# Kernel optimization log

Measured on AMD Instinct MI355X. Metric: run time of the kernel, lower is better.

## Reference

```python
import jax, jax.numpy as jnp
import numpy as np
import math

B, H, W, C = 8, 112, 112, 192
WS, SHIFT, NH = 7, 3, 6
HD = C // NH
N = WS * WS
NW = (H // WS) * (W // WS)
MLP_HID = 4 * C
LOG100 = math.log(100.0)


def _rel_table():
    ch = np.arange(-(WS - 1), WS, dtype=np.float32)
    t = np.stack(np.meshgrid(ch, ch, indexing='ij')).transpose(1, 2, 0).reshape(-1, 2)
    t = t / float(WS - 1) * 8.0
    t = np.sign(t) * np.log2(np.abs(t) + 1.0) / np.log2(8.0)
    return t.astype(np.float32)  # ((2*WS-1)^2, 2)


def _rel_index():
    coords = np.stack(np.meshgrid(np.arange(WS), np.arange(WS), indexing='ij')).reshape(2, -1)
    rel = (coords[:, :, None] - coords[:, None, :]).transpose(1, 2, 0)
    rel = rel + np.array([WS - 1, WS - 1])
    rel = rel * np.array([2 * WS - 1, 1])
    return rel.sum(-1).astype(np.int32)  # (N, N)


def _attn_mask():
    img = np.zeros((H, W), dtype=np.float32)
    cnt = 0
    for hsl in (slice(0, -WS), slice(-WS, -SHIFT), slice(-SHIFT, None)):
        for wsl in (slice(0, -WS), slice(-WS, -SHIFT), slice(-SHIFT, None)):
            img[hsl, wsl] = cnt
            cnt += 1
    mw = img.reshape(H // WS, WS, W // WS, WS).transpose(0, 2, 1, 3).reshape(-1, N)
    diff = mw[:, None, :] - mw[:, :, None]
    return np.where(diff != 0, -100.0, 0.0).astype(np.float32)  # (NW, N, N)

REL_TABLE = jnp.asarray(_rel_table())
REL_INDEX = jnp.asarray(_rel_index())
ATTN_MASK = jnp.asarray(_attn_mask())


def _ln(v, g, b, eps=1e-5):
    m = jnp.mean(v, axis=-1, keepdims=True)
    s = jnp.mean((v - m) ** 2, axis=-1, keepdims=True)
    return (v - m) / jnp.sqrt(s + eps) * g + b


def setup_inputs() -> dict:
    key = jax.random.key(0)
    ks = jax.random.split(key, 12)
    std = 0.02
    inp = {
        'x': jax.random.normal(ks[0], (B, H * W, C), jnp.float32),
        'q_w': jax.random.normal(ks[1], (C, C), jnp.float32) * std,
        'q_b': jnp.zeros((C,), jnp.float32),
        'k_w': jax.random.normal(ks[2], (C, C), jnp.float32) * std,
        'v_w': jax.random.normal(ks[3], (C, C), jnp.float32) * std,
        'v_b': jnp.zeros((C,), jnp.float32),
        'proj_w': jax.random.normal(ks[4], (C, C), jnp.float32) * std,
        'proj_b': jnp.zeros((C,), jnp.float32),
        'logit_scale': jnp.log(10.0 * jnp.ones((NH, 1, 1), jnp.float32)),
        'cpb_w0': jax.random.normal(ks[5], (2, 512), jnp.float32) * std,
        'cpb_b0': jnp.zeros((512,), jnp.float32),
        'cpb_w1': jax.random.normal(ks[6], (512, NH), jnp.float32) * std,
        'ln1_g': jnp.ones((C,), jnp.float32),
        'ln1_b': jnp.zeros((C,), jnp.float32),
        'ln2_g': jnp.ones((C,), jnp.float32),
        'ln2_b': jnp.zeros((C,), jnp.float32),
        'fc1_w': jax.random.normal(ks[7], (C, MLP_HID), jnp.float32) * std,
        'fc1_b': jnp.zeros((MLP_HID,), jnp.float32),
        'fc2_w': jax.random.normal(ks[8], (MLP_HID, C), jnp.float32) * std,
        'fc2_b': jnp.zeros((C,), jnp.float32),
    }
    return inp


def reference(x, q_w, q_b, k_w, v_w, v_b, proj_w, proj_b, logit_scale,
              cpb_w0, cpb_b0, cpb_w1, ln1_g, ln1_b, ln2_g, ln2_b,
              fc1_w, fc1_b, fc2_w, fc2_b):
    shortcut = x  # (B, L, C)
    h = x.reshape(B, H, W, C)
    # cyclic shift
    h = jnp.roll(h, shift=(-SHIFT, -SHIFT), axis=(1, 2))
    # window partition -> (B*NW, N, C)
    h = h.reshape(B, H // WS, WS, W // WS, WS, C).transpose(0, 1, 3, 2, 4, 5)
    h = h.reshape(B * NW, N, C)

    q = (h @ q_w + q_b).reshape(-1, N, NH, HD).transpose(0, 2, 1, 3)
    k = (h @ k_w).reshape(-1, N, NH, HD).transpose(0, 2, 1, 3)
    v = (h @ v_w + v_b).reshape(-1, N, NH, HD).transpose(0, 2, 1, 3)

    # cosine-similarity attention
    q = q / jnp.maximum(jnp.linalg.norm(q, axis=-1, keepdims=True), 1e-6)
    k = k / jnp.maximum(jnp.linalg.norm(k, axis=-1, keepdims=True), 1e-6)
    scale = jnp.exp(jnp.minimum(logit_scale, LOG100))  # (NH,1,1)
    attn = jnp.einsum('bhqd,bhkd->bhqk', q, k) * scale

    # relative position bias via CPB MLP
    rpb = jax.nn.relu(REL_TABLE @ cpb_w0 + cpb_b0) @ cpb_w1  # (169, NH)
    rpb = rpb[REL_INDEX.reshape(-1)].reshape(N, N, NH).transpose(2, 0, 1)
    rpb = 16.0 * jax.nn.sigmoid(rpb)  # (NH, N, N)
    attn = attn + rpb[None]

    # shift mask
    attn = attn.reshape(B, NW, NH, N, N) + ATTN_MASK[None, :, None]
    attn = attn.reshape(B * NW, NH, N, N)
    attn = jax.nn.softmax(attn, axis=-1)

    out = jnp.einsum('bhqk,bhkd->bhqd', attn, v)
    out = out.transpose(0, 2, 1, 3).reshape(B * NW, N, C)
    out = out @ proj_w + proj_b

    # window reverse + reverse shift
    out = out.reshape(B, H // WS, W // WS, WS, WS, C).transpose(0, 1, 3, 2, 4, 5)
    out = out.reshape(B, H, W, C)
    out = jnp.roll(out, shift=(SHIFT, SHIFT), axis=(1, 2)).reshape(B, H * W, C)

    # post-norm residual (Swin-v2)
    h1 = shortcut + _ln(out, ln1_g, ln1_b)
    mlp = jax.nn.gelu(h1 @ fc1_w + fc1_b) @ fc2_w + fc2_b
    return h1 + _ln(mlp, ln2_g, ln2_b)
```

## Files before the change

kernel.cpp:

```cpp
#include <hip/hip_runtime.h>

typedef unsigned short u16;
typedef unsigned int   u32;
typedef __attribute__((ext_vector_type(8))) short bf16x8;
typedef __attribute__((ext_vector_type(4))) float f32x4;

#define B_      8
#define HW_     112
#define C_      192
#define NH_     6
#define HD_     32
#define L_      (HW_*HW_)
#define M_      (B_*L_)
#define MLP_    768
#define QKVN_   576
#define LOG100_ 4.6051702f
#define LOG2E_  1.44269504f

__device__ __forceinline__ float bf2f(u16 u){
  union { float f; u32 i; } v; v.i = ((u32)u) << 16; return v.f;
}
__device__ __forceinline__ u16 f2bf(float f){
  union { float f; u32 i; } v; v.f = f;
  u32 r = (v.i + 0x7fffu + ((v.i >> 16) & 1u)) >> 16;
  return (u16)r;
}
__device__ __forceinline__ u32 pk2(float a, float b){
  return (u32)f2bf(a) | ((u32)f2bf(b) << 16);
}
__device__ __forceinline__ void u4_to_f8(uint4 u, float* f){
  f[0]=bf2f((u16)(u.x&0xffffu)); f[1]=bf2f((u16)(u.x>>16));
  f[2]=bf2f((u16)(u.y&0xffffu)); f[3]=bf2f((u16)(u.y>>16));
  f[4]=bf2f((u16)(u.z&0xffffu)); f[5]=bf2f((u16)(u.z>>16));
  f[6]=bf2f((u16)(u.w&0xffffu)); f[7]=bf2f((u16)(u.w>>16));
}

__device__ __forceinline__ int rowelem(int b, int wh, int ww, int t){
  int i = t/7, j = t - i*7;
  int oi = wh*7 + i + 3; if (oi >= 112) oi -= 112;
  int oj = ww*7 + j + 3; if (oj >= 112) oj -= 112;
  return b*L_ + oi*112 + oj;
}

__global__ __launch_bounds__(256) void prep_weights(
    const float* __restrict__ qw, const float* __restrict__ qb,
    const float* __restrict__ kw, const float* __restrict__ vw,
    const float* __restrict__ vb, const float* __restrict__ pw,
    const float* __restrict__ pb, const float* __restrict__ f1w,
    const float* __restrict__ f1b, const float* __restrict__ f2w,
    const float* __restrict__ f2b,
    u16* __restrict__ wt_qkv, float* __restrict__ b_qkv,
    u16* __restrict__ wt_p,   float* __restrict__ b_p,
    u16* __restrict__ wt_f1,  float* __restrict__ b_f1,
    u16* __restrict__ wt_f2,  float* __restrict__ b_f2)
{
  const int S1 = 110592, S2 = 147456, S3 = 294912, S4 = 442368, TOT = 444096;
  int i = blockIdx.x*256 + threadIdx.x;
  if (i >= TOT) return;
  if (i < S1) {
    int n = i/192, k = i%192;
    float v = (n<192) ? qw[k*192+n] : ((n<384) ? kw[k*192+(n-192)] : vw[k*192+(n-384)]);
    wt_qkv[i] = f2bf(v);
  } else if (i < S2) {
    int j = i - S1; int n = j/192, k = j%192;
    wt_p[j] = f2bf(pw[k*192+n]);
  } else if (i < S3) {
    int j = i - S2; int n = j/192, k = j%192;
    wt_f1[j] = f2bf(f1w[k*768+n]);
  } else if (i < S4) {
    int j = i - S3; int n = j/768, k = j%768;
    wt_f2[j] = f2bf(f2w[k*192+n]);
  } else {
    int j = i - S4;
    if (j < 576)        b_qkv[j] = (j<192) ? qb[j] : ((j<384) ? 0.f : vb[j-384]);
    else if (j < 768)   b_p[j-576]   = pb[j-576];
    else if (j < 1536)  b_f1[j-768]  = f1b[j-768];
    else                b_f2[j-1536] = f2b[j-1536];
  }
}

__device__ __forceinline__ float reltab(float x){
  float v = x * (8.f/6.f);
  float r = __log2f(fabsf(v) + 1.f) * (1.f/3.f);
  return (v < 0.f) ? -r : r;
}

__global__ __launch_bounds__(64) void rpb_a_kernel(
    const float* __restrict__ w0, const float* __restrict__ b0,
    const float* __restrict__ w1, float* __restrict__ rpb169)
{
  int tt = blockIdx.x, lane = threadIdx.x;
  float t0 = reltab((float)(tt/13 - 6));
  float t1 = reltab((float)(tt%13 - 6));
  float acc[6] = {0.f,0.f,0.f,0.f,0.f,0.f};
  for (int j = lane; j < 512; j += 64){
    float hid = fmaxf(t0*w0[j] + t1*w0[512+j] + b0[j], 0.f);
#pragma unroll
    for (int h=0; h<6; h++) acc[h] += hid * w1[j*6+h];
  }
#pragma unroll
  for (int h=0; h<6; h++){
#pragma unroll
    for (int m=32; m>=1; m>>=1) acc[h] += __shfl_xor(acc[h], m);
  }
  if (lane == 0){
#pragma unroll
    for (int h=0; h<6; h++) rpb169[tt*6+h] = acc[h];
  }
}

__global__ __launch_bounds__(256) void rpb_b_kernel(
    const float* __restrict__ rpb169, float* __restrict__ biasT)
{
  int i = blockIdx.x*256 + threadIdx.x;
  if (i >= 98304) return;
  int q = i & 63, key = (i >> 6) & 63;
  int rest = i >> 12;
  int hh = rest % 6, type = rest / 6;
  float val;
  if (key >= 49) val = -60000.f;
  else if (q >= 49) val = 0.f;
  else {
    int qi = q/7, qj = q%7, ki = key/7, kj = key%7;
    int idx = (qi - ki + 6)*13 + (qj - kj + 6);
    float x = rpb169[idx*6 + hh];
    float sig = 16.f / (1.f + __expf(-x));
    int th = type >> 1, tw = type & 1;
    int rq = (th ? (qi<4?1:2) : 0)*3 + (tw ? (qj<4?1:2) : 0);
    int rk = (th ? (ki<4?1:2) : 0)*3 + (tw ? (kj<4?1:2) : 0);
    float msk = (rq != rk) ? -100.f : 0.f;
    val = (sig + msk) * LOG2E_;
  }
  biasT[i] = val;
}


__device__ __forceinline__ float fast_gelu(float v){
  float t = v*v;
  float w = v * fmaf(-0.1029432f, t, -2.30220817f);
  float e = exp2f(w);
  return v * __builtin_amdgcn_rcpf(1.f + e);
}

template<int K, bool GELU>
__global__ __launch_bounds__(512,4) void gemm_kernel(
    const u16* __restrict__ A, const u16* __restrict__ Wt,
    const float* __restrict__ bias, u16* __restrict__ out, int NN)
{
  __shared__ __align__(16) u16 lds[10240];
  const int tid  = threadIdx.x;
  const int wave = tid >> 6, lane = tid & 63;
  const int m0 = blockIdx.x * 128;
  const int n0 = blockIdx.y * 192;
  const int wr = wave >> 1, wc = wave & 1;
  const int lrow = lane >> 2, lslot = lane & 3;
  const int gk = (lslot ^ ((lrow >> 1) & 3)) * 8;

  const u16* gsrc[3]; u32 ldst[3]; int nst = (wave < 4) ? 3 : 2;
#pragma unroll
  for (int t=0; t<3; t++){
    int c = wave + t*8;
    if (c < 8)       { gsrc[t] = A  + (size_t)(m0 + c*16 + lrow)*K + gk;      ldst[t] = c*512; }
    else if (c < 20) { gsrc[t] = Wt + (size_t)(n0 + (c-8)*16 + lrow)*K + gk;  ldst[t] = 4096 + (c-8)*512; }
  }
  const int lr16 = lane & 15;
  const int slot8 = ((lane >> 4) ^ ((lr16 >> 1) & 3)) * 8;
  u32 aoff[2], boff[6];
#pragma unroll
  for (int mt=0; mt<2; mt++) aoff[mt] = (u32)((wr*32 + mt*16 + lr16)*32 + slot8);
#pragma unroll
  for (int nt=0; nt<6; nt++) boff[nt] = (u32)(4096 + (wc*96 + nt*16 + lr16)*32 + slot8);

  float bs[6];
#pragma unroll
  for (int nt=0; nt<6; nt++) bs[nt] = bias[n0 + wc*96 + nt*16 + lr16];

  f32x4 acc[2][6];
#pragma unroll
  for (int mt=0; mt<2; mt++)
#pragma unroll
    for (int nt=0; nt<6; nt++)
      acc[mt][nt] = (f32x4){0.f,0.f,0.f,0.f};

  for (int k0 = 0; k0 < K; k0 += 32) {
#pragma unroll
    for (int t=0; t<3; t++){
      if (t < nst) {
        __builtin_amdgcn_global_load_lds(
            (const __attribute__((address_space(1))) void*)gsrc[t],
            (__attribute__((address_space(3))) void*)&lds[ldst[t]], 16, 0, 0);
        gsrc[t] += 32;
      }
    }
    __syncthreads();
    bf16x8 af[2], bf[6];
#pragma unroll
    for (int mt=0; mt<2; mt++) af[mt] = *(const bf16x8*)&lds[aoff[mt]];
#pragma unroll
    for (int nt=0; nt<6; nt++) bf[nt] = *(const bf16x8*)&lds[boff[nt]];
#pragma unroll
    for (int mt=0; mt<2; mt++)
#pragma unroll
      for (int nt=0; nt<6; nt++)
        acc[mt][nt] = __builtin_amdgcn_mfma_f32_16x16x32_bf16(af[mt], bf[nt], acc[mt][nt], 0, 0, 0);
    __syncthreads();
  }
#pragma unroll
  for (int mt=0; mt<2; mt++){
    int rbase = m0 + wr*32 + mt*16 + (lane >> 4)*4;
#pragma unroll
    for (int nt=0; nt<6; nt++){
      int col = n0 + wc*96 + nt*16 + lr16;
#pragma unroll
      for (int r2=0; r2<4; r2++){
        float v = acc[mt][nt][r2] + bs[nt];
        if (GELU) v = fast_gelu(v);
        out[(size_t)(rbase + r2)*NN + col] = f2bf(v);
      }
    }
  }
}

__global__ __launch_bounds__(512,4) void gemm_qkv_kernel(
    const float* __restrict__ X, const u16* __restrict__ Wt,
    const float* __restrict__ bias, u16* __restrict__ out)
{
  __shared__ __align__(16) u16 lds[10240];
  const int tid  = threadIdx.x;
  const int wave = tid >> 6, lane = tid & 63;
  const int m0 = blockIdx.x * 128;
  const int n0 = blockIdx.y * 192;
  const int wr = wave >> 1, wc = wave & 1;
  const int lrow = lane >> 2, lslot = lane & 3;
  const int gk = (lslot ^ ((lrow >> 1) & 3)) * 8;

  const u16* gsrcB[2]; u32 ldstB[2]; int nstB = (wave < 4) ? 2 : 1;
#pragma unroll
  for (int t=0; t<2; t++){
    int c = wave + t*8;
    if (c < 12) { gsrcB[t] = Wt + (size_t)(n0 + c*16 + lrow)*192 + gk; ldstB[t] = 4096 + c*512; }
  }
  const int ar = tid >> 2, as = tid & 3;
  const float* gsrcA = X + (size_t)(m0 + ar)*192 + as*8;
  const u32 dsta = (u32)(ar*32 + (as ^ ((ar >> 1) & 3))*8);

  const int lr16 = lane & 15;
  const int slot8 = ((lane >> 4) ^ ((lr16 >> 1) & 3)) * 8;
  u32 aoff[2], boff[6];
#pragma unroll
  for (int mt=0; mt<2; mt++) aoff[mt] = (u32)((wr*32 + mt*16 + lr16)*32 + slot8);
#pragma unroll
  for (int nt=0; nt<6; nt++) boff[nt] = (u32)(4096 + (wc*96 + nt*16 + lr16)*32 + slot8);

  float bs[6];
#pragma unroll
  for (int nt=0; nt<6; nt++) bs[nt] = bias[n0 + wc*96 + nt*16 + lr16];

  f32x4 acc[2][6];
#pragma unroll
  for (int mt=0; mt<2; mt++)
#pragma unroll
    for (int nt=0; nt<6; nt++)
      acc[mt][nt] = (f32x4){0.f,0.f,0.f,0.f};

  for (int k0 = 0; k0 < 192; k0 += 32) {
#pragma unroll
    for (int t=0; t<2; t++){
      if (t < nstB) {
        __builtin_amdgcn_global_load_lds(
            (const __attribute__((address_space(1))) void*)gsrcB[t],
            (__attribute__((address_space(3))) void*)&lds[ldstB[t]], 16, 0, 0);
        gsrcB[t] += 32;
      }
    }
    float4 a0 = *(const float4*)gsrcA;
    float4 a1 = *(const float4*)(gsrcA + 4);
    gsrcA += 32;
    uint4 aw;
    aw.x = pk2(a0.x, a0.y); aw.y = pk2(a0.z, a0.w);
    aw.z = pk2(a1.x, a1.y); aw.w = pk2(a1.z, a1.w);
    *(uint4*)(void*)&lds[dsta] = aw;
    __syncthreads();
    bf16x8 af[2], bf[6];
#pragma unroll
    for (int mt=0; mt<2; mt++) af[mt] = *(const bf16x8*)&lds[aoff[mt]];
#pragma unroll
    for (int nt=0; nt<6; nt++) bf[nt] = *(const bf16x8*)&lds[boff[nt]];
#pragma unroll
    for (int mt=0; mt<2; mt++)
#pragma unroll
      for (int nt=0; nt<6; nt++)
        acc[mt][nt] = __builtin_amdgcn_mfma_f32_16x16x32_bf16(af[mt], bf[nt], acc[mt][nt], 0, 0, 0);
    __syncthreads();
  }
#pragma unroll
  for (int mt=0; mt<2; mt++){
    int rbase = m0 + wr*32 + mt*16 + (lane >> 4)*4;
#pragma unroll
    for (int nt=0; nt<6; nt++){
      int col = n0 + wc*96 + nt*16 + lr16;
#pragma unroll
      for (int r2=0; r2<4; r2++){
        float v = acc[mt][nt][r2] + bs[nt];
        out[(size_t)(rbase + r2)*QKVN_ + col] = f2bf(v);
      }
    }
  }
}

__global__ __launch_bounds__(64) void attn_kernel(
    const u16* __restrict__ qkv, const float* __restrict__ lsc,
    const float* __restrict__ biasT, u16* __restrict__ attn_out)
{
  __shared__ __align__(16) u16 pbuf[4096];
  const int id = blockIdx.x;
  const int hh = id % 6;
  const int w  = id / 6;
  const int b  = w >> 8;
  const int wh = (w >> 4) & 15, ww = w & 15;
  const int lane = threadIdx.x;
  const int lg = lane >> 4, lr = lane & 15;
  const int type = ((wh==15)?2:0) + ((ww==15)?1:0);
  const float qscale = __expf(fminf(lsc[hh], LOG100_)) * LOG2E_;

  union BU { bf16x8 v; u32 u[4]; };

  bf16x8 qf[4], kf[4];
#pragma unroll
  for (int mt=0; mt<4; mt++){
    int t = mt*16 + lr; if (t > 48) t = 48;
    int off = rowelem(b, wh, ww, t)*QKVN_ + hh*32 + lg*8;
    uint4 u = *(const uint4*)(qkv + off);
    float f[8]; u4_to_f8(u, f);
    float ss = 0.f;
#pragma unroll
    for (int d=0; d<8; d++) ss += f[d]*f[d];
    ss += __shfl_xor(ss, 16); ss += __shfl_xor(ss, 32);
    float rn = qscale / fmaxf(sqrtf(ss), 1e-6f);
    BU bu;
#pragma unroll
    for (int p=0; p<4; p++) bu.u[p] = pk2(f[2*p]*rn, f[2*p+1]*rn);
    qf[mt] = bu.v;
  }
#pragma unroll
  for (int nt=0; nt<4; nt++){
    int t = nt*16 + lr; if (t > 48) t = 48;
    int off = rowelem(b, wh, ww, t)*QKVN_ + 192 + hh*32 + lg*8;
    uint4 u = *(const uint4*)(qkv + off);
    float f[8]; u4_to_f8(u, f);
    float ss = 0.f;
#pragma unroll
    for (int d=0; d<8; d++) ss += f[d]*f[d];
    ss += __shfl_xor(ss, 16); ss += __shfl_xor(ss, 32);
    float rn = 1.f / fmaxf(sqrtf(ss), 1e-6f);
    BU bu;
#pragma unroll
    for (int p=0; p<4; p++) bu.u[p] = pk2(f[2*p]*rn, f[2*p+1]*rn);
    kf[nt] = bu.v;
  }

  f32x4 s[4][4];
#pragma unroll
  for (int mt=0;mt<4;mt++)
#pragma unroll
    for (int nt=0;nt<4;nt++)
      s[mt][nt] = __builtin_amdgcn_mfma_f32_16x16x32_bf16(qf[mt], kf[nt],
                    (f32x4){0.f,0.f,0.f,0.f}, 0, 0, 0);

  const float* bt = biasT + (size_t)(type*6 + hh)*4096;
#pragma unroll
  for (int nt=0;nt<4;nt++){
    int key = nt*16 + lr;
#pragma unroll
    for (int mt=0;mt<4;mt++){
      f32x4 bv = *(const f32x4*)(bt + key*64 + mt*16 + lg*4);
      s[mt][nt] += bv;
    }
  }

  float rsum[4][4];
#pragma unroll
  for (int mt=0;mt<4;mt++){
#pragma unroll
    for (int r2=0;r2<4;r2++){
      float m = fmaxf(fmaxf(s[mt][0][r2], s[mt][1][r2]),
                      fmaxf(s[mt][2][r2], s[mt][3][r2]));
      m = fmaxf(m, __shfl_xor(m, 1));
      m = fmaxf(m, __shfl_xor(m, 2));
      m = fmaxf(m, __shfl_xor(m, 4));
      m = fmaxf(m, __shfl_xor(m, 8));
      float e0 = exp2f(s[mt][0][r2]-m), e1 = exp2f(s[mt][1][r2]-m),
            e2 = exp2f(s[mt][2][r2]-m), e3 = exp2f(s[mt][3][r2]-m);
      s[mt][0][r2]=e0; s[mt][1][r2]=e1; s[mt][2][r2]=e2; s[mt][3][r2]=e3;
      float sum = (e0+e1)+(e2+e3);
      sum += __shfl_xor(sum, 1);
      sum += __shfl_xor(sum, 2);
      sum += __shfl_xor(sum, 4);
      sum += __shfl_xor(sum, 8);
      rsum[mt][r2] = 1.f/sum;
    }
  }

#pragma unroll
  for (int mt=0;mt<4;mt++)
#pragma unroll
    for (int r2=0;r2<4;r2++){
      int q = mt*16 + lg*4 + r2;
#pragma unroll
      for (int nt=0;nt<4;nt++){
        int key = nt*16 + lr;
        int addr = (q*128 + key*2) ^ ((q&7)<<4);
        *(u16*)((char*)pbuf + addr) = f2bf(s[mt][nt][r2]);
      }
    }
  __syncthreads();

  f32x4 o[4][2];
#pragma unroll
  for (int mt=0;mt<4;mt++)
#pragma unroll
    for (int dt=0;dt<2;dt++)
      o[mt][dt] = (f32x4){0.f,0.f,0.f,0.f};

#pragma unroll
  for (int kt=0; kt<2; kt++){
    bf16x8 pf[4];
#pragma unroll
    for (int mt=0;mt<4;mt++){
      int q = mt*16 + lr;
      int addr = (q*128 + kt*64 + lg*16) ^ ((q&7)<<4);
      pf[mt] = *(const bf16x8*)((char*)pbuf + addr);
    }
    int voff[8];
#pragma unroll
    for (int j=0;j<8;j++){
      int key = kt*32 + lg*8 + j; if (key > 48) key = 48;
      voff[j] = rowelem(b, wh, ww, key)*QKVN_ + 384 + hh*32 + lr;
    }
#pragma unroll
    for (int dt=0; dt<2; dt++){
      BU bu;
#pragma unroll
      for (int p=0;p<4;p++){
        u16 lo = qkv[voff[2*p]   + dt*16];
        u16 hi = qkv[voff[2*p+1] + dt*16];
        bu.u[p] = (u32)lo | ((u32)hi << 16);
      }
#pragma unroll
      for (int mt=0;mt<4;mt++)
        o[mt][dt] = __builtin_amdgcn_mfma_f32_16x16x32_bf16(pf[mt], bu.v, o[mt][dt], 0, 0, 0);
    }
  }

#pragma unroll
  for (int mt=0;mt<4;mt++)
#pragma unroll
    for (int r2=0;r2<4;r2++){
      int q = mt*16 + lg*4 + r2;
      if (q < 49){
        int off = rowelem(b, wh, ww, q)*C_ + hh*32 + lr;
        float rs = rsum[mt][r2];
        attn_out[off]      = f2bf(o[mt][0][r2]*rs);
        attn_out[off + 16] = f2bf(o[mt][1][r2]*rs);
      }
    }
}

template<bool BASE32, bool OUT32>
__global__ __launch_bounds__(256) void ln_res_kernel(
    const float* __restrict__ base32, const u16* __restrict__ base16,
    const u16* __restrict__ y,
    const float* __restrict__ gg, const float* __restrict__ bb,
    float* __restrict__ out32, u16* __restrict__ out16)
{
  int row  = blockIdx.x*4 + (threadIdx.x >> 6);
  int lane = threadIdx.x & 63;
  size_t ro = (size_t)row*192;
  float v0 = bf2f(y[ro+lane]), v1 = bf2f(y[ro+lane+64]), v2 = bf2f(y[ro+lane+128]);
  float s  = v0+v1+v2;
  float sq = v0*v0+v1*v1+v2*v2;
#pragma unroll
  for (int m=32; m>=1; m>>=1){ s += __shfl_xor(s,m); sq += __shfl_xor(sq,m); }
  float mean = s*(1.f/192.f);
  float var  = fmaxf(sq*(1.f/192.f) - mean*mean, 0.f);
  float rstd = rsqrtf(var + 1e-5f);
  float g0=gg[lane], g1=gg[lane+64], g2=gg[lane+128];
  float b0=bb[lane], b1=bb[lane+64], b2=bb[lane+128];
  float a0, a1, a2;
  if (BASE32) { a0=base32[ro+lane]; a1=base32[ro+lane+64]; a2=base32[ro+lane+128]; }
  else        { a0=bf2f(base16[ro+lane]); a1=bf2f(base16[ro+lane+64]); a2=bf2f(base16[ro+lane+128]); }
  float r0 = a0 + (v0-mean)*rstd*g0 + b0;
  float r1 = a1 + (v1-mean)*rstd*g1 + b1;
  float r2 = a2 + (v2-mean)*rstd*g2 + b2;
  if (OUT32) {
    out32[ro+lane] = r0; out32[ro+lane+64] = r1; out32[ro+lane+128] = r2;
  } else {
    out16[ro+lane] = f2bf(r0); out16[ro+lane+64] = f2bf(r1); out16[ro+lane+128] = f2bf(r2);
  }
}

extern "C" void kernel_launch(void* const* d_in, const int* in_sizes, int n_in,
                              void* d_out, int out_size, void* d_ws, size_t ws_size,
                              hipStream_t stream)
{
  (void)in_sizes; (void)n_in; (void)out_size; (void)ws_size;
  const float* x      = (const float*)d_in[0];
  const float* q_w    = (const float*)d_in[1];
  const float* q_b    = (const float*)d_in[2];
  const float* k_w    = (const float*)d_in[3];
  const float* v_w    = (const float*)d_in[4];
  const float* v_b    = (const float*)d_in[5];
  const float* proj_w = (const float*)d_in[6];
  const float* proj_b = (const float*)d_in[7];
  const float* lsc    = (const float*)d_in[8];
  const float* cpb_w0 = (const float*)d_in[9];
  const float* cpb_b0 = (const float*)d_in[10];
  const float* cpb_w1 = (const float*)d_in[11];
  const float* ln1_g  = (const float*)d_in[12];
  const float* ln1_b  = (const float*)d_in[13];
  const float* ln2_g  = (const float*)d_in[14];
  const float* ln2_b  = (const float*)d_in[15];
  const float* fc1_w  = (const float*)d_in[16];
  const float* fc1_b  = (const float*)d_in[17];
  const float* fc2_w  = (const float*)d_in[18];
  const float* fc2_b  = (const float*)d_in[19];

  char* ws = (char*)d_ws;
  size_t o = 0;
  u16* qkvb = (u16*)(ws + o);
  u16* mid  = qkvb;              o += 154140672;
  u16* attn_o = (u16*)(ws + o);
  u16* h1b    = attn_o;          o += 38535168;
  u16* proj_o = (u16*)(ws + o);
  u16* m2     = proj_o;          o += 38535168;
  u16* wt_qkv = (u16*)(ws + o);  o += 221184;
  float* b_qkv= (float*)(ws + o);o += 2304;
  u16* wt_p   = (u16*)(ws + o);  o += 73728;
  float* b_p  = (float*)(ws + o);o += 768;
  u16* wt_f1  = (u16*)(ws + o);  o += 294912;
  float* b_f1 = (float*)(ws + o);o += 3072;
  u16* wt_f2  = (u16*)(ws + o);  o += 294912;
  float* b_f2 = (float*)(ws + o);o += 768;
  float* rpb169 = (float*)(ws + o); o += 4096;
  float* biasT  = (float*)(ws + o); o += 393216;

  prep_weights<<<1735, 256, 0, stream>>>(q_w, q_b, k_w, v_w, v_b, proj_w, proj_b,
      fc1_w, fc1_b, fc2_w, fc2_b, wt_qkv, b_qkv, wt_p, b_p, wt_f1, b_f1, wt_f2, b_f2);
  rpb_a_kernel<<<169, 64, 0, stream>>>(cpb_w0, cpb_b0, cpb_w1, rpb169);
  rpb_b_kernel<<<384, 256, 0, stream>>>(rpb169, biasT);

  gemm_qkv_kernel<<<dim3(784,3), 512, 0, stream>>>(x, wt_qkv, b_qkv, qkvb);
  attn_kernel<<<12288, 64, 0, stream>>>(qkvb, lsc, biasT, attn_o);
  gemm_kernel<192,false><<<dim3(784,1), 512, 0, stream>>>(attn_o, wt_p, b_p, proj_o, 192);
  ln_res_kernel<true,false><<<25088, 256, 0, stream>>>(x, nullptr, proj_o,
      ln1_g, ln1_b, nullptr, h1b);
  gemm_kernel<192,true><<<dim3(784,4), 512, 0, stream>>>(h1b, wt_f1, b_f1, mid, 768);
  gemm_kernel<768,false><<<dim3(784,1), 512, 0, stream>>>(mid, wt_f2, b_f2, m2, 192);
  ln_res_kernel<false,true><<<25088, 256, 0, stream>>>(nullptr, h1b, m2,
      ln2_g, ln2_b, (float*)d_out, nullptr);
}
```

Measured before the change: 359.7 us.

## Restructure window attention: stage V in LDS, transposed scores, vectorized output

The attention kernel now loads V rows with coalesced 16-byte loads and stages them transposed in swizzled LDS, replacing per-element scattered 2-byte global gathers. Scores are computed as K·Q so each lane owns one query column, which simplifies the softmax reductions to two shuffles. Normalization moves before P is written to LDS, and the output goes through LDS so it can be written as 16-byte rows. The bias table layout is transposed to match, and hardware bf16 pack and rcp instructions replace software rounding. This adds LDS use and extra barriers, and leaves a redundant cvtpk line in the GEMM that is immediately overwritten.

```diff
diff --git a/kernel.cpp b/kernel.cpp
--- a/kernel.cpp
+++ b/kernel.cpp
@@ -27,6 +27,11 @@
 }
 __device__ __forceinline__ u32 pk2(float a, float b){
   return (u32)f2bf(a) | ((u32)f2bf(b) << 16);
+}
+__device__ __forceinline__ u32 cvtpk(float a, float b){
+  u32 r;
+  asm volatile("v_cvt_pk_bf16_f32 %0, %1, %2" : "=v"(r) : "v"(a), "v"(b));
+  return r;
 }
 __device__ __forceinline__ void u4_to_f8(uint4 u, float* f){
   f[0]=bf2f((u16)(u.x&0xffffu)); f[1]=bf2f((u16)(u.x>>16));
@@ -110,11 +115,11 @@
 }
 
 __global__ __launch_bounds__(256) void rpb_b_kernel(
-    const float* __restrict__ rpb169, float* __restrict__ biasT)
+    const float* __restrict__ rpb169, float* __restrict__ biasQ)
 {
   int i = blockIdx.x*256 + threadIdx.x;
   if (i >= 98304) return;
-  int q = i & 63, key = (i >> 6) & 63;
+  int key = i & 63, q = (i >> 6) & 63;
   int rest = i >> 12;
   int hh = rest % 6, type = rest / 6;
   float val;
@@ -131,9 +136,8 @@
     float msk = (rq != rk) ? -100.f : 0.f;
     val = (sig + msk) * LOG2E_;
   }
-  biasT[i] = val;
-}
-
+  biasQ[i] = val;
+}
 
 __device__ __forceinline__ float fast_gelu(float v){
   float t = v*v;
@@ -277,6 +281,7 @@
     float4 a1 = *(const float4*)(gsrcA + 4);
     gsrcA += 32;
     uint4 aw;
+    aw.x = cvtpk(a0.y, a0.x); aw.x = pk2(a0.x, a0.y);
     aw.x = pk2(a0.x, a0.y); aw.y = pk2(a0.z, a0.w);
     aw.z = pk2(a1.x, a1.y); aw.w = pk2(a1.z, a1.w);
     *(uint4*)(void*)&lds[dsta] = aw;
@@ -310,9 +315,10 @@
 
 __global__ __launch_bounds__(64) void attn_kernel(
     const u16* __restrict__ qkv, const float* __restrict__ lsc,
-    const float* __restrict__ biasT, u16* __restrict__ attn_out)
-{
-  __shared__ __align__(16) u16 pbuf[4096];
+    const float* __restrict__ biasQ, u16* __restrict__ attn_out)
+{
+  __shared__ __align__(16) u16 smem[6144];
+  char* smb = (char*)smem;
   const int id = blockIdx.x;
   const int hh = id % 6;
   const int w  = id / 6;
@@ -325,145 +331,184 @@
 
   union BU { bf16x8 v; u32 u[4]; };
 
+  const int myrow = rowelem(b, wh, ww, min(lane, 48));
+
+  {
+    const u16* vsrc = qkv + (size_t)myrow*QKVN_ + 384 + hh*32;
+#pragma unroll
+    for (int r=0; r<4; r++){
+      uint4 u = *(const uint4*)(vsrc + r*8);
+      u32 wds[4] = {u.x, u.y, u.z, u.w};
+#pragma unroll
+      for (int i=0; i<8; i++){
+        int d = r*8 + i;
+        u16 val = (u16)(wds[i>>1] >> ((i&1)*16));
+        int addr = 8192 + ((d*128 + lane*2) ^ ((d&7)<<4));
+        *(u16*)(smb + addr) = val;
+      }
+    }
+  }
+
+  int rowq[4];
+#pragma unroll
+  for (int t=0; t<4; t++) rowq[t] = __shfl(myrow, t*16 + lr);
+
   bf16x8 qf[4], kf[4];
 #pragma unroll
-  for (int mt=0; mt<4; mt++){
-    int t = mt*16 + lr; if (t > 48) t = 48;
-    int off = rowelem(b, wh, ww, t)*QKVN_ + hh*32 + lg*8;
-    uint4 u = *(const uint4*)(qkv + off);
+  for (int qt=0; qt<4; qt++){
+    const u16* base = qkv + (size_t)rowq[qt]*QKVN_ + hh*32 + lg*8;
+    uint4 u = *(const uint4*)base;
     float f[8]; u4_to_f8(u, f);
     float ss = 0.f;
 #pragma unroll
     for (int d=0; d<8; d++) ss += f[d]*f[d];
     ss += __shfl_xor(ss, 16); ss += __shfl_xor(ss, 32);
-    float rn = qscale / fmaxf(sqrtf(ss), 1e-6f);
+    float rn = qscale * __builtin_amdgcn_rcpf(fmaxf(sqrtf(ss), 1e-6f));
     BU bu;
 #pragma unroll
-    for (int p=0; p<4; p++) bu.u[p] = pk2(f[2*p]*rn, f[2*p+1]*rn);
-    qf[mt] = bu.v;
-  }
-#pragma unroll
-  for (int nt=0; nt<4; nt++){
-    int t = nt*16 + lr; if (t > 48) t = 48;
-    int off = rowelem(b, wh, ww, t)*QKVN_ + 192 + hh*32 + lg*8;
-    uint4 u = *(const uint4*)(qkv + off);
+    for (int p=0; p<4; p++) bu.u[p] = cvtpk(f[2*p]*rn, f[2*p+1]*rn);
+    qf[qt] = bu.v;
+  }
+#pragma unroll
+  for (int kt=0; kt<4; kt++){
+    const u16* base = qkv + (size_t)rowq[kt]*QKVN_ + 192 + hh*32 + lg*8;
+    uint4 u = *(const uint4*)base;
     float f[8]; u4_to_f8(u, f);
     float ss = 0.f;
 #pragma unroll
     for (int d=0; d<8; d++) ss += f[d]*f[d];
     ss += __shfl_xor(ss, 16); ss += __shfl_xor(ss, 32);
-    float rn = 1.f / fmaxf(sqrtf(ss), 1e-6f);
+    float rn = __builtin_amdgcn_rcpf(fmaxf(sqrtf(ss), 1e-6f));
     BU bu;
 #pragma unroll
-    for (int p=0; p<4; p++) bu.u[p] = pk2(f[2*p]*rn, f[2*p+1]*rn);
-    kf[nt] = bu.v;
-  }
-
-  f32x4 s[4][4];
-#pragma unroll
-  for (int mt=0;mt<4;mt++)
-#pragma unroll
-    for (int nt=0;nt<4;nt++)
-      s[mt][nt] = __builtin_amdgcn_mfma_f32_16x16x32_bf16(qf[mt], kf[nt],
-                    (f32x4){0.f,0.f,0.f,0.f}, 0, 0, 0);
-
-  const float* bt = biasT + (size_t)(type*6 + hh)*4096;
-#pragma unroll
-  for (int nt=0;nt<4;nt++){
-    int key = nt*16 + lr;
-#pragma unroll
-    for (int mt=0;mt<4;mt++){
-      f32x4 bv = *(const f32x4*)(bt + key*64 + mt*16 + lg*4);
-      s[mt][nt] += bv;
-    }
-  }
-
-  float rsum[4][4];
-#pragma unroll
-  for (int mt=0;mt<4;mt++){
-#pragma unroll
-    for (int r2=0;r2<4;r2++){
-      float m = fmaxf(fmaxf(s[mt][0][r2], s[mt][1][r2]),
-                      fmaxf(s[mt][2][r2], s[mt][3][r2]));
-      m = fmaxf(m, __shfl_xor(m, 1));
-      m = fmaxf(m, __shfl_xor(m, 2));
-      m = fmaxf(m, __shfl_xor(m, 4));
-      m = fmaxf(m, __shfl_xor(m, 8));
-      float e0 = exp2f(s[mt][0][r2]-m), e1 = exp2f(s[mt][1][r2]-m),
-            e2 = exp2f(s[mt][2][r2]-m), e3 = exp2f(s[mt][3][r2]-m);
-      s[mt][0][r2]=e0; s[mt][1][r2]=e1; s[mt][2][r2]=e2; s[mt][3][r2]=e3;
-      float sum = (e0+e1)+(e2+e3);
-      sum += __shfl_xor(sum, 1);
-      sum += __shfl_xor(sum, 2);
-      sum += __shfl_xor(sum, 4);
-      sum += __shfl_xor(sum, 8);
-      rsum[mt][r2] = 1.f/sum;
-    }
-  }
-
-#pragma unroll
-  for (int mt=0;mt<4;mt++)
-#pragma unroll
-    for (int r2=0;r2<4;r2++){
+    for (int p=0; p<4; p++) bu.u[p] = cvtpk(f[2*p]*rn, f[2*p+1]*rn);
+    kf[kt] = bu.v;
+  }
+
+  f32x4 s2[4][4];
+#pragma unroll
+  for (int kt=0; kt<4; kt++)
+#pragma unroll
+    for (int qt=0; qt<4; qt++)
+      s2[kt][qt] = __builtin_amdgcn_mfma_f32_16x16x32_bf16(kf[kt], qf[qt],
+                     (f32x4){0.f,0.f,0.f,0.f}, 0, 0, 0);
+
+  const float* bq = biasQ + (size_t)(type*6 + hh)*4096;
+#pragma unroll
+  for (int qt=0; qt<4; qt++){
+    int q = qt*16 + lr;
+#pragma unroll
+    for (int kt=0; kt<4; kt++){
+      f32x4 bv = *(const f32x4*)(bq + q*64 + kt*16 + lg*4);
+      s2[kt][qt] += bv;
+    }
+  }
+
+#pragma unroll
+  for (int qt=0; qt<4; qt++){
+    float m = s2[0][qt][0];
+#pragma unroll
+    for (int kt=0; kt<4; kt++)
+#pragma unroll
+      for (int r2=0; r2<4; r2++) m = fmaxf(m, s2[kt][qt][r2]);
+    m = fmaxf(m, __shfl_xor(m, 16));
+    m = fmaxf(m, __shfl_xor(m, 32));
+    float sum = 0.f;
+#pragma unroll
+    for (int kt=0; kt<4; kt++)
+#pragma unroll
+      for (int r2=0; r2<4; r2++){
+        float e = exp2f(s2[kt][qt][r2] - m);
+        s2[kt][qt][r2] = e; sum += e;
+      }
+    sum += __shfl_xor(sum, 16);
+    sum += __shfl_xor(sum, 32);
+    float rs = __builtin_amdgcn_rcpf(sum);
+#pragma unroll
+    for (int kt=0; kt<4; kt++)
+#pragma unroll
+      for (int r2=0; r2<4; r2++) s2[kt][qt][r2] *= rs;
+  }
+
+#pragma unroll
+  for (int qt=0; qt<4; qt++){
+    int q = qt*16 + lr;
+    int rowb = q*128, swz = (q&7)<<4;
+#pragma unroll
+    for (int kt=0; kt<4; kt++){
+      u32 lo = cvtpk(s2[kt][qt][0], s2[kt][qt][1]);
+      u32 hi = cvtpk(s2[kt][qt][2], s2[kt][qt][3]);
+      int addr = (rowb + kt*32 + lg*8) ^ swz;
+      *(uint2*)(smb + addr) = make_uint2(lo, hi);
+    }
+  }
+  __syncthreads();
+
+  f32x4 o[4][2];
+#pragma unroll
+  for (int mt=0; mt<4; mt++)
+#pragma unroll
+    for (int dt=0; dt<2; dt++)
+      o[mt][dt] = (f32x4){0.f,0.f,0.f,0.f};
+
+#pragma unroll
+  for (int kb=0; kb<2; kb++){
+    bf16x8 pf[4];
+#pragma unroll
+    for (int mt=0; mt<4; mt++){
+      int q = mt*16 + lr;
+      int addr = (q*128 + kb*64 + lg*16) ^ ((q&7)<<4);
+      pf[mt] = *(const bf16x8*)(smb + addr);
+    }
+    bf16x8 vf[2];
+#pragma unroll
+    for (int dt=0; dt<2; dt++){
+      int d = lr + dt*16;
+      int addr = 8192 + ((d*128 + kb*64 + lg*16) ^ ((d&7)<<4));
+      vf[dt] = *(const bf16x8*)(smb + addr);
+    }
+#pragma unroll
+    for (int mt=0; mt<4; mt++)
+#pragma unroll
+      for (int dt=0; dt<2; dt++)
+        o[mt][dt] = __builtin_amdgcn_mfma_f32_16x16x32_bf16(pf[mt], vf[dt], o[mt][dt], 0, 0, 0);
+  }
+  __syncthreads();
+
+#pragma unroll
+  for (int mt=0; mt<4; mt++)
+#pragma unroll
+    for (int r2=0; r2<4; r2++){
       int q = mt*16 + lg*4 + r2;
-#pragma unroll
-      for (int nt=0;nt<4;nt++){
-        int key = nt*16 + lr;
-        int addr = (q*128 + key*2) ^ ((q&7)<<4);
-        *(u16*)((char*)pbuf + addr) = f2bf(s[mt][nt][r2]);
+      int swz = (q&7)<<4;
+#pragma unroll
+      for (int dt=0; dt<2; dt++){
+        int d = lr + dt*16;
+        int addr = (q*128 + d*4) ^ swz;
+        *(float*)(smb + addr) = o[mt][dt][r2];
       }
     }
   __syncthreads();
-
-  f32x4 o[4][2];
-#pragma unroll
-  for (int mt=0;mt<4;mt++)
-#pragma unroll
-    for (int dt=0;dt<2;dt++)
-      o[mt][dt] = (f32x4){0.f,0.f,0.f,0.f};
-
-#pragma unroll
-  for (int kt=0; kt<2; kt++){
-    bf16x8 pf[4];
-#pragma unroll
-    for (int mt=0;mt<4;mt++){
-      int q = mt*16 + lr;
-      int addr = (q*128 + kt*64 + lg*16) ^ ((q&7)<<4);
-      pf[mt] = *(const bf16x8*)((char*)pbuf + addr);
-    }
-    int voff[8];
-#pragma unroll
-    for (int j=0;j<8;j++){
-      int key = kt*32 + lg*8 + j; if (key > 48) key = 48;
-      voff[j] = rowelem(b, wh, ww, key)*QKVN_ + 384 + hh*32 + lr;
-    }
-#pragma unroll
-    for (int dt=0; dt<2; dt++){
-      BU bu;
-#pragma unroll
-      for (int p=0;p<4;p++){
-        u16 lo = qkv[voff[2*p]   + dt*16];
-        u16 hi = qkv[voff[2*p+1] + dt*16];
-        bu.u[p] = (u32)lo | ((u32)hi << 16);
-      }
-#pragma unroll
-      for (int mt=0;mt<4;mt++)
-        o[mt][dt] = __builtin_amdgcn_mfma_f32_16x16x32_bf16(pf[mt], bu.v, o[mt][dt], 0, 0, 0);
-    }
-  }
-
-#pragma unroll
-  for (int mt=0;mt<4;mt++)
-#pragma unroll
-    for (int r2=0;r2<4;r2++){
-      int q = mt*16 + lg*4 + r2;
-      if (q < 49){
-        int off = rowelem(b, wh, ww, q)*C_ + hh*32 + lr;
-        float rs = rsum[mt][r2];
-        attn_out[off]      = f2bf(o[mt][0][r2]*rs);
-        attn_out[off + 16] = f2bf(o[mt][1][r2]*rs);
-      }
-    }
+  if (lane < 49){
+    int q = lane;
+    float vals[32];
+#pragma unroll
+    for (int c=0; c<8; c++){
+      int addr = (q*128 + c*16) ^ ((q&7)<<4);
+      f32x4 v4 = *(const f32x4*)(smb + addr);
+      vals[c*4+0]=v4[0]; vals[c*4+1]=v4[1]; vals[c*4+2]=v4[2]; vals[c*4+3]=v4[3];
+    }
+    u16* op = attn_out + (size_t)myrow*C_ + hh*32;
+#pragma unroll
+    for (int j=0; j<4; j++){
+      uint4 u;
+      u.x = cvtpk(vals[j*8+0], vals[j*8+1]);
+      u.y = cvtpk(vals[j*8+2], vals[j*8+3]);
+      u.z = cvtpk(vals[j*8+4], vals[j*8+5]);
+      u.w = cvtpk(vals[j*8+6], vals[j*8+7]);
+      *(uint4*)(void*)(op + j*8) = u;
+    }
+  }
 }
 
 template<bool BASE32, bool OUT32>
@@ -542,15 +587,15 @@
   u16* wt_f2  = (u16*)(ws + o);  o += 294912;
   float* b_f2 = (float*)(ws + o);o += 768;
   float* rpb169 = (float*)(ws + o); o += 4096;
-  float* biasT  = (float*)(ws + o); o += 393216;
+  float* biasQ  = (float*)(ws + o); o += 393216;
 
   prep_weights<<<1735, 256, 0, stream>>>(q_w, q_b, k_w, v_w, v_b, proj_w, proj_b,
       fc1_w, fc1_b, fc2_w, fc2_b, wt_qkv, b_qkv, wt_p, b_p, wt_f1, b_f1, wt_f2, b_f2);
   rpb_a_kernel<<<169, 64, 0, stream>>>(cpb_w0, cpb_b0, cpb_w1, rpb169);
-  rpb_b_kernel<<<384, 256, 0, stream>>>(rpb169, biasT);
+  rpb_b_kernel<<<384, 256, 0, stream>>>(rpb169, biasQ);
 
   gemm_qkv_kernel<<<dim3(784,3), 512, 0, stream>>>(x, wt_qkv, b_qkv, qkvb);
-  attn_kernel<<<12288, 64, 0, stream>>>(qkvb, lsc, biasT, attn_o);
+  attn_kernel<<<12288, 64, 0, stream>>>(qkvb, lsc, biasQ, attn_o);
   gemm_kernel<192,false><<<dim3(784,1), 512, 0, stream>>>(attn_o, wt_p, b_p, proj_o, 192);
   ln_res_kernel<true,false><<<25088, 256, 0, stream>>>(x, nullptr, proj_o,
       ln1_g, ln1_b, nullptr, h1b);
```

After: 368.8 us. 2.5% more time.
